# Performance work log

Hardware: AMD Instinct MI355X
Metric: run time of the kernel (lower is better)

The kernel has to match this reference:

```python
import jax, jax.numpy as jnp
import numpy as np

W_POINT = 1.0
W_COEFF = 0.5
W_AFFINE = 0.5


def _euler_xyz_to_matrix(angles):
    # angles: [B, 3] Euler angles, XYZ convention: R = Rx @ Ry @ Rz (pytorch3d style)
    ax, ay, az = angles[:, 0], angles[:, 1], angles[:, 2]
    cx, sx = jnp.cos(ax), jnp.sin(ax)
    cy, sy = jnp.cos(ay), jnp.sin(ay)
    cz, sz = jnp.cos(az), jnp.sin(az)
    one = jnp.ones_like(cx)
    zero = jnp.zeros_like(cx)
    Rx = jnp.stack([one, zero, zero,
                    zero, cx, -sx,
                    zero, sx, cx], axis=-1).reshape(-1, 3, 3)
    Ry = jnp.stack([cy, zero, sy,
                    zero, one, zero,
                    -sy, zero, cy], axis=-1).reshape(-1, 3, 3)
    Rz = jnp.stack([cz, -sz, zero,
                    sz, cz, zero,
                    zero, zero, one], axis=-1).reshape(-1, 3, 3)
    return Rx @ Ry @ Rz


def _chamfer(pred, targ):
    # pred: [B,N,3], targ: [B,M,3]; symmetric chamfer of squared distances
    p2 = jnp.sum(pred * pred, axis=-1)        # [B,N]
    t2 = jnp.sum(targ * targ, axis=-1)        # [B,M]
    d2 = p2[:, :, None] + t2[:, None, :] - 2.0 * jnp.einsum('bnd,bmd->bnm', pred, targ)
    d2 = jnp.maximum(d2, 0.0)
    return jnp.mean(jnp.min(d2, axis=2)) + jnp.mean(jnp.min(d2, axis=1))


def setup_inputs() -> dict:
    key = jax.random.key(0)
    ks = jax.random.split(key, 6)
    B, N, M, K = 16, 4096, 4096, 128
    return {
        'pred_shape': jax.random.normal(ks[0], (B, N, 3), dtype=jnp.float32),
        'pred_weights': jax.random.normal(ks[1], (B, K), dtype=jnp.float32),
        'pred_affine': jax.random.uniform(ks[2], (B, 9), dtype=jnp.float32),
        'targ_shape': jax.random.normal(ks[3], (B, M, 3), dtype=jnp.float32),
        'targ_weights': jax.random.normal(ks[4], (B, K), dtype=jnp.float32),
        'targ_affine': jax.random.uniform(ks[5], (B, 9), dtype=jnp.float32),
    }


def reference(pred_shape, pred_weights, pred_affine, targ_shape, targ_weights, targ_affine):
    rot, trans, scale = targ_affine[:, 0:3], targ_affine[:, 3:6], targ_affine[:, 6:9]
    R = _euler_xyz_to_matrix(rot)                                   # [B,3,3]
    # row-vector convention (pytorch3d Transform3d): p' = (p @ R) * s + t
    targ_moving = jnp.einsum('bmd,bde->bme', targ_shape, R) * scale[:, None, :] + trans[:, None, :]
    point_loss = _chamfer(pred_shape, targ_moving)
    coeff_loss = jnp.mean((pred_weights - targ_weights) ** 2)
    affine_loss = jnp.mean((pred_affine - targ_affine) ** 2)
    total = W_POINT * point_loss + W_COEFF * coeff_loss + W_AFFINE * affine_loss
    return total, point_loss, coeff_loss, affine_loss
```

## Files before the change

kernel.cpp:

```cpp
#include <hip/hip_runtime.h>
#include <math.h>

#define BB 16
#define NN 4096
#define KK 128
#define RT 2048
#define CT 128
#define RPT 8
#define TPB 256
#define NRTILE (NN / RT)
#define NCTILE (NN / CT)
#define W_POINT  1.0f
#define W_COEFF  0.5f
#define W_AFFINE 0.5f

__device__ inline float min3f(float a, float b, float c) {
    float r;
    asm("v_min3_f32 %0, %1, %2, %3" : "=v"(r) : "v"(a), "v"(b), "v"(c));
    return r;
}

__device__ inline void compute_affine(const float* __restrict__ aff,
                                      float R[9], float sc[3], float tr[3]) {
    float ax = aff[0], ay = aff[1], az = aff[2];
    tr[0] = aff[3]; tr[1] = aff[4]; tr[2] = aff[5];
    sc[0] = aff[6]; sc[1] = aff[7]; sc[2] = aff[8];
    float cx = cosf(ax), sx = sinf(ax);
    float cy = cosf(ay), sy = sinf(ay);
    float cz = cosf(az), sz = sinf(az);
    R[0] = cy * cz;                 R[1] = -cy * sz;                R[2] = sy;
    R[3] = cx * sz + sx * sy * cz;  R[4] = cx * cz - sx * sy * sz;  R[5] = -sx * cy;
    R[6] = sx * sz - cx * sy * cz;  R[7] = sx * cz + cx * sy * sz;  R[8] = cx * cy;
}

__device__ inline void apply_affine(const float R[9], const float sc[3], const float tr[3],
                                    float x, float y, float z,
                                    float& ox, float& oy, float& oz) {
    ox = fmaf(fmaf(x, R[0], fmaf(y, R[3], z * R[6])), sc[0], tr[0]);
    oy = fmaf(fmaf(x, R[1], fmaf(y, R[4], z * R[7])), sc[1], tr[1]);
    oz = fmaf(fmaf(x, R[2], fmaf(y, R[5], z * R[8])), sc[2], tr[2]);
}

__global__ __launch_bounds__(TPB, 4) void chamfer_kernel(
        const float* __restrict__ pred_shape,
        const float* __restrict__ targ_shape,
        const float* __restrict__ targ_affine,
        unsigned int* __restrict__ pmin) {
    __shared__ float4 ldsc[CT];

    const int bx    = blockIdx.x;
    const int ctile = bx & (NCTILE - 1);
    const int rtile = (bx >> 5) & (NRTILE - 1);
    const int b     = bx >> 6;
    const int tid   = threadIdx.x;
    const int lane  = tid & 63;

    float R[9], sc[3], tr[3];
    compute_affine(targ_affine + b * 9, R, sc, tr);

    if (tid < CT) {
        const float* t = targ_shape + ((size_t)b * NN + ctile * CT + tid) * 3;
        float mx, my, mz;
        apply_affine(R, sc, tr, t[0], t[1], t[2], mx, my, mz);
        ldsc[tid] = make_float4(mx, my, mz, fmaf(mx, mx, fmaf(my, my, mz * mz)));
    }

    const int rowbase = rtile * RT;
    float ax[RPT], ay[RPT], az[RPT], q2[RPT], rmin[RPT];
    #pragma unroll
    for (int k = 0; k < RPT; ++k) {
        const float* p = pred_shape + ((size_t)b * NN + rowbase + k * TPB + tid) * 3;
        float x = p[0], y = p[1], z = p[2];
        q2[k] = fmaf(x, x, fmaf(y, y, z * z));
        ax[k] = -2.0f * x; ay[k] = -2.0f * y; az[k] = -2.0f * z;
        rmin[k] = 1e30f;
    }
    __syncthreads();

    float cr0 = 1e30f, cr1 = 1e30f;
    const int rot = ((lane + 1) & 63) << 2;
    for (int i = 0; i < 64; ++i) {
        const int idx = (lane + i) & 63;
        float4 t0 = ldsc[idx];
        float4 t1 = ldsc[idx + 64];
        float da[RPT], db[RPT];
        #pragma unroll
        for (int k = 0; k < RPT; ++k) {
            float s0 = q2[k] + t0.w;
            float s1 = q2[k] + t1.w;
            float e0 = fmaf(ax[k], t0.x, fmaf(ay[k], t0.y, fmaf(az[k], t0.z, s0)));
            float e1 = fmaf(ax[k], t1.x, fmaf(ay[k], t1.y, fmaf(az[k], t1.z, s1)));
            rmin[k] = min3f(rmin[k], e0, e1);
            da[k] = e0; db[k] = e1;
        }
        float a0 = min3f(da[0], da[1], da[2]);
        float b0 = min3f(da[3], da[4], da[5]);
        float c0 = min3f(da[6], da[7], cr0);
        cr0 = min3f(a0, b0, c0);
        float a1 = min3f(db[0], db[1], db[2]);
        float b1 = min3f(db[3], db[4], db[5]);
        float c1 = min3f(db[6], db[7], cr1);
        cr1 = min3f(a1, b1, c1);
        cr0 = __int_as_float(__builtin_amdgcn_ds_bpermute(rot, __float_as_int(cr0)));
        cr1 = __int_as_float(__builtin_amdgcn_ds_bpermute(rot, __float_as_int(cr1)));
    }

    #pragma unroll
    for (int k = 0; k < RPT; ++k) {
        float d = fmaxf(rmin[k], 0.0f);
        atomicMin(&pmin[(size_t)b * NN + rowbase + k * TPB + tid],
                  __float_as_uint(d));
    }
    {
        float d0 = fmaxf(cr0, 0.0f);
        atomicMin(&pmin[(size_t)(BB + b) * NN + ctile * CT + lane],
                  __float_as_uint(d0));
        float d1 = fmaxf(cr1, 0.0f);
        atomicMin(&pmin[(size_t)(BB + b) * NN + ctile * CT + 64 + lane],
                  __float_as_uint(d1));
    }
}

__global__ __launch_bounds__(TPB) void reduce_pmin(
        const unsigned int* __restrict__ pmin,
        float* __restrict__ partials) {
    const int tid = threadIdx.x;
    const uint4* pm4 = (const uint4*)(pmin + (size_t)blockIdx.x * 4096);
    float ps = 0.0f;
    #pragma unroll
    for (int r = 0; r < 4; ++r) {
        uint4 u = pm4[r * TPB + tid];
        ps += __uint_as_float(u.x) + __uint_as_float(u.y)
            + __uint_as_float(u.z) + __uint_as_float(u.w);
    }
    #pragma unroll
    for (int off = 32; off > 0; off >>= 1) ps += __shfl_down(ps, off);
    __shared__ float sps[4];
    const int wid = tid >> 6;
    if ((tid & 63) == 0) sps[wid] = ps;
    __syncthreads();
    if (tid == 0) partials[blockIdx.x] = sps[0] + sps[1] + sps[2] + sps[3];
}

__global__ __launch_bounds__(TPB) void final_combine(
        const float* __restrict__ partials,
        const float* __restrict__ pred_w,  const float* __restrict__ targ_w,
        const float* __restrict__ pred_aff, const float* __restrict__ targ_aff,
        float* __restrict__ out) {
    const int tid = threadIdx.x;
    float ps = (tid < 32) ? partials[tid] : 0.0f;
    float cs = 0.0f;
    #pragma unroll
    for (int r = 0; r < (BB * KK) / TPB; ++r) {
        float d = pred_w[r * TPB + tid] - targ_w[r * TPB + tid];
        cs = fmaf(d, d, cs);
    }
    float as = 0.0f;
    if (tid < BB * 9) {
        float d = pred_aff[tid] - targ_aff[tid];
        as = d * d;
    }
    #pragma unroll
    for (int off = 32; off > 0; off >>= 1) {
        ps += __shfl_down(ps, off);
        cs += __shfl_down(cs, off);
        as += __shfl_down(as, off);
    }
    __shared__ float sps[4], scs[4], sas[4];
    const int wid = tid >> 6;
    if ((tid & 63) == 0) { sps[wid] = ps; scs[wid] = cs; sas[wid] = as; }
    __syncthreads();
    if (tid == 0) {
        float p = sps[0] + sps[1] + sps[2] + sps[3];
        float c = scs[0] + scs[1] + scs[2] + scs[3];
        float a = sas[0] + sas[1] + sas[2] + sas[3];
        float point  = p / (float)(BB * NN);
        float coeff  = c / (float)(BB * KK);
        float affine = a / (float)(BB * 9);
        out[0] = W_POINT * point + W_COEFF * coeff + W_AFFINE * affine;
        out[1] = point;
        out[2] = coeff;
        out[3] = affine;
    }
}

extern "C" void kernel_launch(void* const* d_in, const int* in_sizes, int n_in,
                              void* d_out, int out_size, void* d_ws, size_t ws_size,
                              hipStream_t stream) {
    const float* pred_shape = (const float*)d_in[0];
    const float* pred_w     = (const float*)d_in[1];
    const float* pred_aff   = (const float*)d_in[2];
    const float* targ_shape = (const float*)d_in[3];
    const float* targ_w     = (const float*)d_in[4];
    const float* targ_aff   = (const float*)d_in[5];
    float* out = (float*)d_out;
    unsigned int* pmin = (unsigned int*)d_ws;
    float* partials = (float*)(pmin + 2 * BB * NN);

    hipMemsetAsync(pmin, 0x7f, (size_t)2 * BB * NN * sizeof(unsigned int), stream);

    chamfer_kernel<<<dim3(BB * NRTILE * NCTILE), TPB, 0, stream>>>(
        pred_shape, targ_shape, targ_aff, pmin);
    reduce_pmin<<<32, TPB, 0, stream>>>(pmin, partials);
    final_combine<<<1, TPB, 0, stream>>>(partials, pred_w, targ_w,
                                         pred_aff, targ_aff, out);
}
```

Before: 101.9 us.

## Use packed f32 math in chamfer inner loop and replace atomics with partial buffers

The inner distance loop now uses v_pk_fma_f32/v_pk_add_f32 on pairs of target points, with a structure-of-arrays LDS layout that interleaves the two column halves. The aim is to halve the VALU instruction count for the distance computation. The memset and atomicMin reductions are replaced by writing per-tile partial minima to workspace buffers, which a 48-block reduce kernel then min-reduces and sums. This costs more workspace memory and more global traffic in the reduction: 32 column tiles are scanned per row, which is a sizeable read.

```diff
diff --git a/kernel.cpp b/kernel.cpp
--- a/kernel.cpp
+++ b/kernel.cpp
@@ -14,9 +14,21 @@
 #define W_COEFF  0.5f
 #define W_AFFINE 0.5f
 
+typedef float f2 __attribute__((ext_vector_type(2)));
+
 __device__ inline float min3f(float a, float b, float c) {
     float r;
     asm("v_min3_f32 %0, %1, %2, %3" : "=v"(r) : "v"(a), "v"(b), "v"(c));
+    return r;
+}
+__device__ inline f2 pk_add(f2 a, f2 b) {
+    f2 r;
+    asm("v_pk_add_f32 %0, %1, %2" : "=v"(r) : "v"(a), "v"(b));
+    return r;
+}
+__device__ inline f2 pk_fma(f2 a, f2 b, f2 c) {
+    f2 r;
+    asm("v_pk_fma_f32 %0, %1, %2, %3" : "=v"(r) : "v"(a), "v"(b), "v"(c));
     return r;
 }
 
@@ -45,8 +57,9 @@
         const float* __restrict__ pred_shape,
         const float* __restrict__ targ_shape,
         const float* __restrict__ targ_affine,
-        unsigned int* __restrict__ pmin) {
-    __shared__ float4 ldsc[CT];
+        float* __restrict__ rp,
+        float* __restrict__ cp) {
+    __shared__ float ldsb[4 * CT];
 
     const int bx    = blockIdx.x;
     const int ctile = bx & (NCTILE - 1);
@@ -54,92 +67,118 @@
     const int b     = bx >> 6;
     const int tid   = threadIdx.x;
     const int lane  = tid & 63;
-
-    float R[9], sc[3], tr[3];
-    compute_affine(targ_affine + b * 9, R, sc, tr);
+    const int wid   = tid >> 6;
 
     if (tid < CT) {
+        float R[9], sc[3], tr[3];
+        compute_affine(targ_affine + b * 9, R, sc, tr);
+        const int s = tid & 63, h = tid >> 6;
         const float* t = targ_shape + ((size_t)b * NN + ctile * CT + tid) * 3;
         float mx, my, mz;
         apply_affine(R, sc, tr, t[0], t[1], t[2], mx, my, mz);
-        ldsc[tid] = make_float4(mx, my, mz, fmaf(mx, mx, fmaf(my, my, mz * mz)));
+        ldsb[0 * CT + 2 * s + h] = mx;
+        ldsb[1 * CT + 2 * s + h] = my;
+        ldsb[2 * CT + 2 * s + h] = mz;
+        ldsb[3 * CT + 2 * s + h] = fmaf(mx, mx, fmaf(my, my, mz * mz));
     }
 
     const int rowbase = rtile * RT;
-    float ax[RPT], ay[RPT], az[RPT], q2[RPT], rmin[RPT];
+    f2 axp[RPT], ayp[RPT], azp[RPT], q2p[RPT];
+    float rmin[RPT];
     #pragma unroll
     for (int k = 0; k < RPT; ++k) {
         const float* p = pred_shape + ((size_t)b * NN + rowbase + k * TPB + tid) * 3;
         float x = p[0], y = p[1], z = p[2];
-        q2[k] = fmaf(x, x, fmaf(y, y, z * z));
-        ax[k] = -2.0f * x; ay[k] = -2.0f * y; az[k] = -2.0f * z;
+        float q2 = fmaf(x, x, fmaf(y, y, z * z));
+        axp[k] = (f2){-2.0f * x, -2.0f * x};
+        ayp[k] = (f2){-2.0f * y, -2.0f * y};
+        azp[k] = (f2){-2.0f * z, -2.0f * z};
+        q2p[k] = (f2){q2, q2};
         rmin[k] = 1e30f;
     }
     __syncthreads();
 
-    float cr0 = 1e30f, cr1 = 1e30f;
+    const f2* base = (const f2*)ldsb;
+    f2 cr = (f2){1e30f, 1e30f};
     const int rot = ((lane + 1) & 63) << 2;
+    int idx = lane;
     for (int i = 0; i < 64; ++i) {
-        const int idx = (lane + i) & 63;
-        float4 t0 = ldsc[idx];
-        float4 t1 = ldsc[idx + 64];
-        float da[RPT], db[RPT];
+        f2 x01 = base[idx];
+        f2 y01 = base[64 + idx];
+        f2 z01 = base[128 + idx];
+        f2 w01 = base[192 + idx];
+        float cA, cB;
         #pragma unroll
-        for (int k = 0; k < RPT; ++k) {
-            float s0 = q2[k] + t0.w;
-            float s1 = q2[k] + t1.w;
-            float e0 = fmaf(ax[k], t0.x, fmaf(ay[k], t0.y, fmaf(az[k], t0.z, s0)));
-            float e1 = fmaf(ax[k], t1.x, fmaf(ay[k], t1.y, fmaf(az[k], t1.z, s1)));
-            rmin[k] = min3f(rmin[k], e0, e1);
-            da[k] = e0; db[k] = e1;
+        for (int k = 0; k < RPT; k += 2) {
+            f2 s0 = pk_add(q2p[k], w01);
+            f2 e0 = pk_fma(azp[k], z01, s0);
+            e0 = pk_fma(ayp[k], y01, e0);
+            e0 = pk_fma(axp[k], x01, e0);
+            f2 s1 = pk_add(q2p[k + 1], w01);
+            f2 e1 = pk_fma(azp[k + 1], z01, s1);
+            e1 = pk_fma(ayp[k + 1], y01, e1);
+            e1 = pk_fma(axp[k + 1], x01, e1);
+            rmin[k]     = min3f(rmin[k],     e0[0], e0[1]);
+            rmin[k + 1] = min3f(rmin[k + 1], e1[0], e1[1]);
+            if (k == 0) {
+                cA = min3f(e0[0], e1[0], cr[0]);
+                cB = min3f(e0[1], e1[1], cr[1]);
+            } else {
+                cA = min3f(cA, e0[0], e1[0]);
+                cB = min3f(cB, e0[1], e1[1]);
+            }
         }
-        float a0 = min3f(da[0], da[1], da[2]);
-        float b0 = min3f(da[3], da[4], da[5]);
-        float c0 = min3f(da[6], da[7], cr0);
-        cr0 = min3f(a0, b0, c0);
-        float a1 = min3f(db[0], db[1], db[2]);
-        float b1 = min3f(db[3], db[4], db[5]);
-        float c1 = min3f(db[6], db[7], cr1);
-        cr1 = min3f(a1, b1, c1);
-        cr0 = __int_as_float(__builtin_amdgcn_ds_bpermute(rot, __float_as_int(cr0)));
-        cr1 = __int_as_float(__builtin_amdgcn_ds_bpermute(rot, __float_as_int(cr1)));
-    }
-
-    #pragma unroll
-    for (int k = 0; k < RPT; ++k) {
-        float d = fmaxf(rmin[k], 0.0f);
-        atomicMin(&pmin[(size_t)b * NN + rowbase + k * TPB + tid],
-                  __float_as_uint(d));
-    }
+        cr[0] = __int_as_float(__builtin_amdgcn_ds_bpermute(rot, __float_as_int(cA)));
+        cr[1] = __int_as_float(__builtin_amdgcn_ds_bpermute(rot, __float_as_int(cB)));
+        idx = (idx + 1) & 63;
+    }
+
+    #pragma unroll
+    for (int k = 0; k < RPT; ++k)
+        rp[((size_t)b * NCTILE + ctile) * NN + rowbase + k * TPB + tid] =
+            fmaxf(rmin[k], 0.0f);
     {
-        float d0 = fmaxf(cr0, 0.0f);
-        atomicMin(&pmin[(size_t)(BB + b) * NN + ctile * CT + lane],
-                  __float_as_uint(d0));
-        float d1 = fmaxf(cr1, 0.0f);
-        atomicMin(&pmin[(size_t)(BB + b) * NN + ctile * CT + 64 + lane],
-                  __float_as_uint(d1));
-    }
-}
-
-__global__ __launch_bounds__(TPB) void reduce_pmin(
-        const unsigned int* __restrict__ pmin,
+        float* cbase = cp + (((size_t)b * NRTILE + rtile) * 4 + wid) * NN + ctile * CT;
+        cbase[lane]      = fmaxf(cr[0], 0.0f);
+        cbase[64 + lane] = fmaxf(cr[1], 0.0f);
+    }
+}
+
+__global__ __launch_bounds__(TPB) void reduce_kernel(
+        const float* __restrict__ rp, const float* __restrict__ cp,
         float* __restrict__ partials) {
+    const int j = blockIdx.x;
     const int tid = threadIdx.x;
-    const uint4* pm4 = (const uint4*)(pmin + (size_t)blockIdx.x * 4096);
-    float ps = 0.0f;
-    #pragma unroll
-    for (int r = 0; r < 4; ++r) {
-        uint4 u = pm4[r * TPB + tid];
-        ps += __uint_as_float(u.x) + __uint_as_float(u.y)
-            + __uint_as_float(u.z) + __uint_as_float(u.w);
-    }
-    #pragma unroll
-    for (int off = 32; off > 0; off >>= 1) ps += __shfl_down(ps, off);
+    float sum = 0.0f;
+    if (j < 32) {
+        #pragma unroll
+        for (int r8 = 0; r8 < 8; ++r8) {
+            const int gr = j * 2048 + r8 * TPB + tid;
+            const int b = gr >> 12, row = gr & (NN - 1);
+            const float* basep = rp + (size_t)b * NCTILE * NN + row;
+            float m = basep[0];
+            #pragma unroll 4
+            for (int c = 1; c < NCTILE; ++c) m = fminf(m, basep[(size_t)c * NN]);
+            sum += m;
+        }
+    } else {
+        const int b = j - 32;
+        #pragma unroll
+        for (int c16 = 0; c16 < 16; ++c16) {
+            const int col = c16 * TPB + tid;
+            const float* basep = cp + (size_t)b * 8 * NN + col;
+            float m = basep[0];
+            #pragma unroll
+            for (int s = 1; s < 8; ++s) m = fminf(m, basep[(size_t)s * NN]);
+            sum += m;
+        }
+    }
+    #pragma unroll
+    for (int off = 32; off > 0; off >>= 1) sum += __shfl_down(sum, off);
     __shared__ float sps[4];
-    const int wid = tid >> 6;
-    if ((tid & 63) == 0) sps[wid] = ps;
+    if ((tid & 63) == 0) sps[tid >> 6] = sum;
     __syncthreads();
-    if (tid == 0) partials[blockIdx.x] = sps[0] + sps[1] + sps[2] + sps[3];
+    if (tid == 0) partials[j] = sps[0] + sps[1] + sps[2] + sps[3];
 }
 
 __global__ __launch_bounds__(TPB) void final_combine(
@@ -148,7 +187,7 @@
         const float* __restrict__ pred_aff, const float* __restrict__ targ_aff,
         float* __restrict__ out) {
     const int tid = threadIdx.x;
-    float ps = (tid < 32) ? partials[tid] : 0.0f;
+    float ps = (tid < 48) ? partials[tid] : 0.0f;
     float cs = 0.0f;
     #pragma unroll
     for (int r = 0; r < (BB * KK) / TPB; ++r) {
@@ -194,14 +233,14 @@
     const float* targ_w     = (const float*)d_in[4];
     const float* targ_aff   = (const float*)d_in[5];
     float* out = (float*)d_out;
-    unsigned int* pmin = (unsigned int*)d_ws;
-    float* partials = (float*)(pmin + 2 * BB * NN);
-
-    hipMemsetAsync(pmin, 0x7f, (size_t)2 * BB * NN * sizeof(unsigned int), stream);
+
+    float* rp = (float*)d_ws;
+    float* cp = rp + (size_t)BB * NCTILE * NN;
+    float* partials = cp + (size_t)BB * 8 * NN;
 
     chamfer_kernel<<<dim3(BB * NRTILE * NCTILE), TPB, 0, stream>>>(
-        pred_shape, targ_shape, targ_aff, pmin);
-    reduce_pmin<<<32, TPB, 0, stream>>>(pmin, partials);
+        pred_shape, targ_shape, targ_aff, rp, cp);
+    reduce_kernel<<<48, TPB, 0, stream>>>(rp, cp, partials);
     final_combine<<<1, TPB, 0, stream>>>(partials, pred_w, targ_w,
                                          pred_aff, targ_aff, out);
 }
```

New measurement: 147.1 us. 44.4% more time.
